# Kernel tuning notes

Hardware: AMD Instinct MI355X
Metric: run time of the kernel (lower is better)

Reference implementation:

```python
import jax, jax.numpy as jnp
import numpy as np

# init kwargs (constants of the module)
SF = 0.05          # quantization scale factor
GROUP_SIZE = 8     # values per group sharing a term budget
NUM_EXPS = 12      # max number of power-of-two terms kept per group
MAXBITS = 8        # bit-width of the quantized integer magnitude


def setup_inputs() -> dict:
    key = jax.random.key(0)
    x = jax.random.normal(key, (4096, 4096), dtype=jnp.float32)
    return {"x": x}


def _radix2_mod_group(x):
    qmax = 2 ** MAXBITS - 1
    # uniform quantization to signed integers
    q = jnp.clip(jnp.round(x / SF), -qmax, qmax).astype(jnp.int32)
    sign = jnp.sign(q)
    mag = jnp.abs(q)
    g = mag.reshape(-1, GROUP_SIZE)                       # [G, gs]
    exps = jnp.arange(MAXBITS, dtype=jnp.int32)           # [B]
    bits = (g[..., None] >> exps) & 1                     # [G, gs, B] radix-2 terms
    # candidate terms: exponent where the bit is set, -1 otherwise
    cand = jnp.where(bits == 1, exps, -1).reshape(-1, GROUP_SIZE * MAXBITS)
    # keep the NUM_EXPS largest-exponent terms in each group (ties -> lowest index)
    _, idx = jax.lax.top_k(cand, NUM_EXPS)                # [G, NUM_EXPS]
    gidx = jnp.arange(cand.shape[0])[:, None]
    keep = jnp.zeros_like(cand).at[gidx, idx].set(1)      # [G, gs*B]
    keep = keep.reshape(-1, GROUP_SIZE, MAXBITS) * bits   # mask out slots with no term
    recon = jnp.sum(keep << exps, axis=-1)                # [G, gs] kept-term magnitude
    recon = recon * sign.reshape(-1, GROUP_SIZE)
    return (recon.astype(x.dtype) * jnp.asarray(SF, x.dtype)).reshape(x.shape)


def reference(x):
    return _radix2_mod_group(x)
```

## Files before the change

### kernel.cpp

```cpp
#include <hip/hip_runtime.h>


constexpr float SF = 0.05f;
constexpr float RCP = 20.0f;
constexpr int NUM_EXPS = 12;

__device__ __forceinline__ unsigned long long transpose8x8(unsigned long long x) {
  unsigned long long t;
  t = (x ^ (x >> 7)) & 0x00AA00AA00AA00AAull; x ^= t ^ (t << 7);
  t = (x ^ (x >> 14)) & 0x0000CCCC0000CCCCull; x ^= t ^ (t << 14);
  t = (x ^ (x >> 28)) & 0x00000000F0F0F0F0ull; x ^= t ^ (t << 28);
  return x;
}

__device__ __forceinline__ void process_group(const float v[8], float o[8]) {
  unsigned long long M = 0ull;
#pragma unroll
  for (int i = 0; i < 8; ++i) {
    float m  = __builtin_fabsf(v[i]);
    float q0 = m * RCP;
    float r0 = __builtin_fmaf(-SF, q0, m);
    float q  = __builtin_fmaf(r0, RCP, q0);
    float r  = fminf(rintf(q), 255.0f);
    unsigned mi = (unsigned)r;
    M |= (unsigned long long)mi << (8 * (7 - i));
  }

  unsigned long long w = transpose8x8(M);

  int P = __popcll(w);
  int jj = P > NUM_EXPS ? P - NUM_EXPS : 0;

  unsigned long long xx = w;
  int pos = 0;
  int c;
  c = __popcll(xx & 0xffffffffull);
  { int s = (jj >= c); pos += s << 5; jj -= s ? c : 0; xx = s ? (xx >> 32) : xx; }
  c = __popc((unsigned)xx & 0xffffu);
  { int s = (jj >= c); pos += s << 4; jj -= s ? c : 0; xx = s ? (xx >> 16) : xx; }
  c = __popc((unsigned)xx & 0xffu);
  { int s = (jj >= c); pos += s << 3; jj -= s ? c : 0; xx = s ? (xx >> 8) : xx; }
  c = __popc((unsigned)xx & 0xfu);
  { int s = (jj >= c); pos += s << 2; jj -= s ? c : 0; xx = s ? (xx >> 4) : xx; }
  c = __popc((unsigned)xx & 0x3u);
  { int s = (jj >= c); pos += s << 1; jj -= s ? c : 0; xx = s ? (xx >> 2) : xx; }
  c = (int)((unsigned)xx & 1u);
  { int s = (jj >= c); pos += s; }

  unsigned long long keep = w & (~0ull << pos);

  unsigned long long Kt = transpose8x8(keep);

#pragma unroll
  for (int i = 0; i < 8; ++i) {
    unsigned mi = (unsigned)(Kt >> (8 * (7 - i))) & 0xffu;
    o[i] = copysignf((float)mi * SF, v[i]);
  }
}

__global__ __launch_bounds__(256) void radix2_mod_group_kernel(
    const float4* __restrict__ xv, float4* __restrict__ ov) {
  int t = blockIdx.x * blockDim.x + threadIdx.x;

  float4 a0 = xv[4 * t + 0];
  float4 a1 = xv[4 * t + 1];
  float4 a2 = xv[4 * t + 2];
  float4 a3 = xv[4 * t + 3];

  float v0[8] = {a0.x, a0.y, a0.z, a0.w, a1.x, a1.y, a1.z, a1.w};
  float v1[8] = {a2.x, a2.y, a2.z, a2.w, a3.x, a3.y, a3.z, a3.w};

  float o0[8], o1[8];
  process_group(v0, o0);
  ov[4 * t + 0] = make_float4(o0[0], o0[1], o0[2], o0[3]);
  ov[4 * t + 1] = make_float4(o0[4], o0[5], o0[6], o0[7]);
  process_group(v1, o1);
  ov[4 * t + 2] = make_float4(o1[0], o1[1], o1[2], o1[3]);
  ov[4 * t + 3] = make_float4(o1[4], o1[5], o1[6], o1[7]);
}

extern "C" void kernel_launch(void* const* d_in, const int* in_sizes, int n_in,
                              void* d_out, int out_size, void* d_ws, size_t ws_size,
                              hipStream_t stream) {
  const float* x = (const float*)d_in[0];
  float* out = (float*)d_out;
  int n = in_sizes[0];
  int nthreads = n / 16;
  int block = 256;
  int grid = nthreads / block;
  radix2_mod_group_kernel<<<grid, block, 0, stream>>>(
      (const float4*)x, (float4*)out);
}
```

Before: 117.7 us.

## Coalesce loads and stores with wave shuffles, one group per thread

Each thread now handles one 8-value group instead of two. A wavefront loads 128 contiguous float4s with fully coalesced lane-strided accesses, then redistributes them to per-thread groups with cross-lane shuffles, and reverses the shuffle before the coalesced stores. This targets the strided per-thread 64-byte access pattern of the old kernel, at the cost of 32 shuffles per thread, twice as many threads and less ILP per thread.

Measured after the change: 109.0 us. 7.4% less time.

```diff
diff --git a/kernel.cpp b/kernel.cpp
--- a/kernel.cpp
+++ b/kernel.cpp
@@ -61,22 +61,72 @@
 __global__ __launch_bounds__(256) void radix2_mod_group_kernel(
     const float4* __restrict__ xv, float4* __restrict__ ov) {
   int t = blockIdx.x * blockDim.x + threadIdx.x;
+  int lane = threadIdx.x & 63;
+  int wid = t >> 6;
 
-  float4 a0 = xv[4 * t + 0];
-  float4 a1 = xv[4 * t + 1];
-  float4 a2 = xv[4 * t + 2];
-  float4 a3 = xv[4 * t + 3];
+  const float4* ibase = xv + (size_t)wid * 128;
+  float4* obase = ov + (size_t)wid * 128;
 
-  float v0[8] = {a0.x, a0.y, a0.z, a0.w, a1.x, a1.y, a1.z, a1.w};
-  float v1[8] = {a2.x, a2.y, a2.z, a2.w, a3.x, a3.y, a3.z, a3.w};
+  float4 rA = ibase[lane];
+  float4 rB = ibase[64 + lane];
 
-  float o0[8], o1[8];
-  process_group(v0, o0);
-  ov[4 * t + 0] = make_float4(o0[0], o0[1], o0[2], o0[3]);
-  ov[4 * t + 1] = make_float4(o0[4], o0[5], o0[6], o0[7]);
-  process_group(v1, o1);
-  ov[4 * t + 2] = make_float4(o1[0], o1[1], o1[2], o1[3]);
-  ov[4 * t + 3] = make_float4(o1[4], o1[5], o1[6], o1[7]);
+  int s0 = (2 * lane) & 63;
+  int s1 = s0 + 1;
+  bool lo = (lane < 32);
+
+  float v[8];
+  {
+    float ax = __shfl(rA.x, s0), bx = __shfl(rB.x, s0);
+    float ay = __shfl(rA.y, s0), by = __shfl(rB.y, s0);
+    float az = __shfl(rA.z, s0), bz = __shfl(rB.z, s0);
+    float aw = __shfl(rA.w, s0), bw = __shfl(rB.w, s0);
+    v[0] = lo ? ax : bx;
+    v[1] = lo ? ay : by;
+    v[2] = lo ? az : bz;
+    v[3] = lo ? aw : bw;
+  }
+  {
+    float ax = __shfl(rA.x, s1), bx = __shfl(rB.x, s1);
+    float ay = __shfl(rA.y, s1), by = __shfl(rB.y, s1);
+    float az = __shfl(rA.z, s1), bz = __shfl(rB.z, s1);
+    float aw = __shfl(rA.w, s1), bw = __shfl(rB.w, s1);
+    v[4] = lo ? ax : bx;
+    v[5] = lo ? ay : by;
+    v[6] = lo ? az : bz;
+    v[7] = lo ? aw : bw;
+  }
+
+  float o[8];
+  process_group(v, o);
+
+  int m1 = lane >> 1;
+  int m2 = 32 + m1;
+  bool hi = (lane & 1);
+
+  float4 S1, S2;
+  {
+    float l0 = __shfl(o[0], m1), h0 = __shfl(o[4], m1);
+    float l1 = __shfl(o[1], m1), h1 = __shfl(o[5], m1);
+    float l2 = __shfl(o[2], m1), h2 = __shfl(o[6], m1);
+    float l3 = __shfl(o[3], m1), h3 = __shfl(o[7], m1);
+    S1.x = hi ? h0 : l0;
+    S1.y = hi ? h1 : l1;
+    S1.z = hi ? h2 : l2;
+    S1.w = hi ? h3 : l3;
+  }
+  {
+    float l0 = __shfl(o[0], m2), h0 = __shfl(o[4], m2);
+    float l1 = __shfl(o[1], m2), h1 = __shfl(o[5], m2);
+    float l2 = __shfl(o[2], m2), h2 = __shfl(o[6], m2);
+    float l3 = __shfl(o[3], m2), h3 = __shfl(o[7], m2);
+    S2.x = hi ? h0 : l0;
+    S2.y = hi ? h1 : l1;
+    S2.z = hi ? h2 : l2;
+    S2.w = hi ? h3 : l3;
+  }
+
+  obase[lane] = S1;
+  obase[64 + lane] = S2;
 }
 
 extern "C" void kernel_launch(void* const* d_in, const int* in_sizes, int n_in,
@@ -85,9 +135,9 @@
   const float* x = (const float*)d_in[0];
   float* out = (float*)d_out;
   int n = in_sizes[0];
-  int nthreads = n / 16;
+  int ngroups = n / 8;
   int block = 256;
-  int grid = nthreads / block;
+  int grid = ngroups / block;
   radix2_mod_group_kernel<<<grid, block, 0, stream>>>(
       (const float4*)x, (float4*)out);
 }
```

## Split each group across two lanes with shuffle for coalesced float4 access

Applied to the files above, without the earlier changes.

Each thread now handles one float4 instead of two full groups, and the two halves of an 8-value group are combined through a lane shuffle. Both lanes redundantly run the bit-transpose and term selection, then each keeps its own half. Memory access becomes contiguous per lane, so loads and stores coalesce, and there are four times as many threads. The cost is duplicated selection arithmetic and a cross-lane shuffle per group.

Result: faster. 109.5 us (-7.0%).

```diff
diff --git a/kernel.cpp b/kernel.cpp
--- a/kernel.cpp
+++ b/kernel.cpp
@@ -13,23 +13,36 @@
   return x;
 }
 
-__device__ __forceinline__ void process_group(const float v[8], float o[8]) {
-  unsigned long long M = 0ull;
+__global__ __launch_bounds__(256) void radix2_mod_group_kernel(
+    const float4* __restrict__ xv, float4* __restrict__ ov) {
+  int t = blockIdx.x * blockDim.x + threadIdx.x;
+  int p = t & 1;
+
+  float4 a = xv[t];
+  float v[4] = {a.x, a.y, a.z, a.w};
+
+  unsigned P = 0u;
 #pragma unroll
-  for (int i = 0; i < 8; ++i) {
-    float m  = __builtin_fabsf(v[i]);
+  for (int k = 0; k < 4; ++k) {
+    float m  = __builtin_fabsf(v[k]);
     float q0 = m * RCP;
     float r0 = __builtin_fmaf(-SF, q0, m);
     float q  = __builtin_fmaf(r0, RCP, q0);
     float r  = fminf(rintf(q), 255.0f);
     unsigned mi = (unsigned)r;
-    M |= (unsigned long long)mi << (8 * (7 - i));
+    P |= mi << (24 - 8 * k);
   }
+
+  unsigned Q = (unsigned)__shfl_xor((int)P, 1);
+
+  unsigned hi = p ? Q : P;
+  unsigned lo = p ? P : Q;
+  unsigned long long M = ((unsigned long long)hi << 32) | lo;
 
   unsigned long long w = transpose8x8(M);
 
-  int P = __popcll(w);
-  int jj = P > NUM_EXPS ? P - NUM_EXPS : 0;
+  int Pc = __popcll(w);
+  int jj = Pc > NUM_EXPS ? Pc - NUM_EXPS : 0;
 
   unsigned long long xx = w;
   int pos = 0;
@@ -51,32 +64,16 @@
 
   unsigned long long Kt = transpose8x8(keep);
 
+  unsigned my = (unsigned)(Kt >> (p ? 0 : 32));
+
+  float o[4];
 #pragma unroll
-  for (int i = 0; i < 8; ++i) {
-    unsigned mi = (unsigned)(Kt >> (8 * (7 - i))) & 0xffu;
-    o[i] = copysignf((float)mi * SF, v[i]);
+  for (int k = 0; k < 4; ++k) {
+    unsigned mi = (my >> (24 - 8 * k)) & 0xffu;
+    o[k] = copysignf((float)mi * SF, v[k]);
   }
-}
 
-__global__ __launch_bounds__(256) void radix2_mod_group_kernel(
-    const float4* __restrict__ xv, float4* __restrict__ ov) {
-  int t = blockIdx.x * blockDim.x + threadIdx.x;
-
-  float4 a0 = xv[4 * t + 0];
-  float4 a1 = xv[4 * t + 1];
-  float4 a2 = xv[4 * t + 2];
-  float4 a3 = xv[4 * t + 3];
-
-  float v0[8] = {a0.x, a0.y, a0.z, a0.w, a1.x, a1.y, a1.z, a1.w};
-  float v1[8] = {a2.x, a2.y, a2.z, a2.w, a3.x, a3.y, a3.z, a3.w};
-
-  float o0[8], o1[8];
-  process_group(v0, o0);
-  ov[4 * t + 0] = make_float4(o0[0], o0[1], o0[2], o0[3]);
-  ov[4 * t + 1] = make_float4(o0[4], o0[5], o0[6], o0[7]);
-  process_group(v1, o1);
-  ov[4 * t + 2] = make_float4(o1[0], o1[1], o1[2], o1[3]);
-  ov[4 * t + 3] = make_float4(o1[4], o1[5], o1[6], o1[7]);
+  ov[t] = make_float4(o[0], o[1], o[2], o[3]);
 }
 
 extern "C" void kernel_launch(void* const* d_in, const int* in_sizes, int n_in,
@@ -85,7 +82,7 @@
   const float* x = (const float*)d_in[0];
   float* out = (float*)d_out;
   int n = in_sizes[0];
-  int nthreads = n / 16;
+  int nthreads = n / 4;
   int block = 256;
   int grid = nthreads / block;
   radix2_mod_group_kernel<<<grid, block, 0, stream>>>(
```
